# Kernel optimization log

Hardware: AMD Instinct MI355X
Metric: run time of the kernel (lower is better)

## Reference

```python
import jax, jax.numpy as jnp
import numpy as np

N, E, G = 50000, 400000, 64
IN_C, HID, OUT_C, HEADS = 256, 128, 256, 4
LRELU_SLOPE = 0.2
LN_EPS = 1e-5


def setup_inputs() -> dict:
    key = jax.random.key(0)
    ks = jax.random.split(key, 16)
    d = {}
    d["x"] = jax.random.normal(ks[0], (N, IN_C), dtype=jnp.float32)
    d["edge_index"] = jax.random.randint(ks[1], (2, E), 0, N, dtype=jnp.int32)
    d["batch"] = jnp.sort(jax.random.randint(ks[2], (N,), 0, G, dtype=jnp.int32))
    s1 = 1.0 / np.sqrt(IN_C)
    d["W1"] = jax.random.uniform(ks[3], (IN_C, HEADS * HID), jnp.float32, -s1, s1)
    d["att_src1"] = jax.random.normal(ks[4], (HEADS, HID), jnp.float32) * 0.1
    d["att_dst1"] = jax.random.normal(ks[5], (HEADS, HID), jnp.float32) * 0.1
    d["b1"] = jnp.zeros((HEADS * HID,), jnp.float32)
    d["ln1_g"] = jnp.ones((HEADS * HID,), jnp.float32)
    d["ln1_b"] = jnp.zeros((HEADS * HID,), jnp.float32)
    s2 = 1.0 / np.sqrt(HEADS * HID)
    d["W2"] = jax.random.uniform(ks[6], (HEADS * HID, OUT_C), jnp.float32, -s2, s2)
    d["att_src2"] = jax.random.normal(ks[7], (1, OUT_C), jnp.float32) * 0.1
    d["att_dst2"] = jax.random.normal(ks[8], (1, OUT_C), jnp.float32) * 0.1
    d["b2"] = jnp.zeros((OUT_C,), jnp.float32)
    d["ln2_g"] = jnp.ones((OUT_C,), jnp.float32)
    d["ln2_b"] = jnp.zeros((OUT_C,), jnp.float32)
    return d


def _layernorm(x, g, b):
    mu = jnp.mean(x, axis=-1, keepdims=True)
    var = jnp.mean(jnp.square(x - mu), axis=-1, keepdims=True)
    return (x - mu) * jax.lax.rsqrt(var + LN_EPS) * g + b


def _gat_conv(x, src, dst, W, a_src, a_dst, bias):
    # PyG GATConv (eval mode, dropout inactive), self-loops already in src/dst.
    H, C = a_src.shape
    h = (x @ W).reshape(N, H, C)                       # [N,H,C]
    e_src = jnp.einsum('nhc,hc->nh', h, a_src)          # [N,H]
    e_dst = jnp.einsum('nhc,hc->nh', h, a_dst)
    e = jax.nn.leaky_relu(e_src[src] + e_dst[dst], LRELU_SLOPE)  # [Etot,H]
    m = jax.ops.segment_max(e, dst, num_segments=N)     # segment softmax over incoming edges
    ex = jnp.exp(e - m[dst])
    s = jax.ops.segment_sum(ex, dst, num_segments=N)
    alpha = ex / (s[dst] + 1e-16)                       # [Etot,H]
    msg = h[src] * alpha[:, :, None]                    # [Etot,H,C]
    out = jax.ops.segment_sum(msg, dst, num_segments=N) # [N,H,C]
    return out.reshape(N, H * C) + bias


def reference(x, edge_index, batch, W1, att_src1, att_dst1, b1, ln1_g, ln1_b,
              W2, att_src2, att_dst2, b2, ln2_g, ln2_b):
    loops = jnp.arange(N, dtype=edge_index.dtype)
    src = jnp.concatenate([edge_index[0], loops])
    dst = jnp.concatenate([edge_index[1], loops])
    h = _gat_conv(x, src, dst, W1, att_src1, att_dst1, b1)
    h = _layernorm(h, ln1_g, ln1_b)
    h = jax.nn.relu(h)                                  # dropout is identity in eval
    h = _gat_conv(h, src, dst, W2, att_src2, att_dst2, b2)
    h = _layernorm(h, ln2_g, ln2_b)
    # global_mean_pool over graphs
    sums = jax.ops.segment_sum(h, batch, num_segments=G)
    cnts = jax.ops.segment_sum(jnp.ones((N,), h.dtype), batch, num_segments=G)
    return sums / jnp.maximum(cnts, 1.0)[:, None]
```

## Files before the change

### kernel.cpp

```cpp
#include <hip/hip_runtime.h>
#include <hip/hip_bf16.h>
#include <cstdint>

#define LRELU_SLOPE 0.2f

typedef short bf16x8 __attribute__((ext_vector_type(8)));
typedef float f32x4  __attribute__((ext_vector_type(4)));

__device__ __forceinline__ float b2f(unsigned short u) {
  return __uint_as_float(((unsigned int)u) << 16);
}
__device__ __forceinline__ unsigned short f2b(float f) {
  unsigned int u = __float_as_uint(f);
  return (unsigned short)((u + 0x7fff + ((u >> 16) & 1)) >> 16);
}

__device__ __forceinline__ void gload16(const void* g, void* l) {
  __builtin_amdgcn_global_load_lds(
      (const __attribute__((address_space(1))) unsigned int*)g,
      (__attribute__((address_space(3))) unsigned int*)l, 16, 0, 0);
}

__global__ __launch_bounds__(256)
void cvt_bf16_pad(const float* __restrict__ x, unsigned short* __restrict__ o,
                  int M, int D, int Mpad) {
  const int i = blockIdx.x * 256 + threadIdx.x;
  const int per_row = D / 4;
  if (i >= Mpad * per_row) return;
  const int row = i / per_row;
  const int c4  = (i % per_row) * 4;
  ushort4 v = make_ushort4(0, 0, 0, 0);
  if (row < M) {
    const float4 f = *(const float4*)&x[(size_t)row * D + c4];
    v = make_ushort4(f2b(f.x), f2b(f.y), f2b(f.z), f2b(f.w));
  }
  *(ushort4*)&o[(size_t)row * D + c4] = v;
}

__global__ __launch_bounds__(256)
void cvt_wt(const float* __restrict__ W, unsigned short* __restrict__ WT,
            int K, int N) {
  const int j = blockIdx.x * 256 + threadIdx.x;
  if (j >= N * K) return;
  const int n = j / K, k = j % K;
  WT[j] = f2b(W[(size_t)k * N + n]);
}

__global__ __launch_bounds__(256)
void csr_count(const int* __restrict__ ei, int E, int Etot,
               int* __restrict__ count) {
  const int i = blockIdx.x * 256 + threadIdx.x;
  if (i >= Etot) return;
  const int d = (i < E) ? ei[E + i] : (i - E);
  atomicAdd(&count[d], 1);
}

__global__ __launch_bounds__(256)
void scan_blocksum(const int* __restrict__ count, int* __restrict__ bsum, int Nn) {
  const int i0 = blockIdx.x * 1024 + threadIdx.x * 4;
  int s = 0;
#pragma unroll
  for (int k = 0; k < 4; ++k) { const int i = i0 + k; if (i < Nn) s += count[i]; }
#pragma unroll
  for (int off = 1; off < 64; off <<= 1) s += __shfl_xor(s, off);
  __shared__ int ws[4];
  if ((threadIdx.x & 63) == 0) ws[threadIdx.x >> 6] = s;
  __syncthreads();
  if (threadIdx.x == 0) bsum[blockIdx.x] = ws[0] + ws[1] + ws[2] + ws[3];
}

__global__ __launch_bounds__(64)
void scan_top(const int* __restrict__ bsum, int* __restrict__ boff,
              int* __restrict__ rowptrN, int nb) {
  const int t = threadIdx.x;
  const int v = (t < nb) ? bsum[t] : 0;
  int incl = v;
#pragma unroll
  for (int off = 1; off < 64; off <<= 1) {
    const int u = __shfl_up(incl, off);
    if (t >= off) incl += u;
  }
  if (t < nb) boff[t] = incl - v;
  if (t == 63) *rowptrN = incl;
}

__global__ __launch_bounds__(256)
void scan_apply(const int* __restrict__ count, const int* __restrict__ boff,
                int* __restrict__ rowptr, int* __restrict__ cursor, int Nn) {
  const int t = threadIdx.x;
  const int lane = t & 63;
  const int w = t >> 6;
  const int i0 = blockIdx.x * 1024 + t * 4;
  int c[4]; int s = 0;
#pragma unroll
  for (int k = 0; k < 4; ++k) { const int i = i0 + k; c[k] = (i < Nn) ? count[i] : 0; s += c[k]; }
  int incl = s;
#pragma unroll
  for (int off = 1; off < 64; off <<= 1) {
    const int u = __shfl_up(incl, off);
    if (lane >= off) incl += u;
  }
  __shared__ int ws[4];
  if (lane == 63) ws[w] = incl;
  __syncthreads();
  int woff = 0;
  for (int k = 0; k < w; ++k) woff += ws[k];
  int base = boff[blockIdx.x] + woff + incl - s;
#pragma unroll
  for (int k = 0; k < 4; ++k) {
    const int i = i0 + k;
    if (i < Nn) { rowptr[i] = base; cursor[i] = base; base += c[k]; }
  }
}

__global__ __launch_bounds__(256)
void csr_scatter(const int* __restrict__ ei, int E, int Etot,
                 int* __restrict__ cursor, int* __restrict__ srcs) {
  const int i = blockIdx.x * 256 + threadIdx.x;
  if (i >= Etot) return;
  const int s = (i < E) ? ei[i]     : (i - E);
  const int d = (i < E) ? ei[E + i] : (i - E);
  const int pos = atomicAdd(&cursor[d], 1);
  srcs[pos] = s;
}

template<int KSTEPS>
__global__ __launch_bounds__(256)
void gemm_bf16(const unsigned short* __restrict__ A,
               const unsigned short* __restrict__ BT,
               unsigned short* __restrict__ C, int M, int Nn, int K) {
  __shared__ unsigned short As[128 * 32];
  __shared__ unsigned short Bs[128 * 32];
  const int tid  = threadIdx.x;
  const int lane = tid & 63;
  const int wave = tid >> 6;
  const int wm = wave >> 1, wn = wave & 1;
  const int brow = blockIdx.y * 128;
  const int bcol = blockIdx.x * 128;
  const int srow  = tid >> 2;
  const int sslot = tid & 3;
  const int sswz  = sslot ^ (srow & 3);
  const size_t aBase0 = (size_t)(brow + srow) * K + sswz * 8;
  const size_t aBase1 = (size_t)(brow + 64 + srow) * K + sswz * 8;
  const size_t bBase0 = (size_t)(bcol + srow) * K + sswz * 8;
  const size_t bBase1 = (size_t)(bcol + 64 + srow) * K + sswz * 8;
  unsigned short* ldsA0 = &As[srow * 32 + sslot * 8];
  unsigned short* ldsA1 = &As[(64 + srow) * 32 + sslot * 8];
  unsigned short* ldsB0 = &Bs[srow * 32 + sslot * 8];
  unsigned short* ldsB1 = &Bs[(64 + srow) * 32 + sslot * 8];

  f32x4 acc[4][4] = {};
  const int u   = lane >> 4;
  const int r15 = lane & 15;
  const int sw  = u ^ (r15 & 3);

  for (int ks = 0; ks < KSTEPS; ++ks) {
    const int k0 = ks * 32;
    __syncthreads();
    gload16(A + aBase0 + k0, ldsA0);
    gload16(A + aBase1 + k0, ldsA1);
    gload16(BT + bBase0 + k0, ldsB0);
    gload16(BT + bBase1 + k0, ldsB1);
    asm volatile("s_waitcnt vmcnt(0)" ::: "memory");
    __syncthreads();
    bf16x8 af[4], bfv[4];
#pragma unroll
    for (int m = 0; m < 4; ++m) {
      const int row = wm * 64 + m * 16 + r15;
      af[m]  = *(const bf16x8*)&As[row * 32 + sw * 8];
      const int col = wn * 64 + m * 16 + r15;
      bfv[m] = *(const bf16x8*)&Bs[col * 32 + sw * 8];
    }
#pragma unroll
    for (int m = 0; m < 4; ++m)
#pragma unroll
      for (int n = 0; n < 4; ++n)
        acc[m][n] = __builtin_amdgcn_mfma_f32_16x16x32_bf16(
            af[m], bfv[n], acc[m][n], 0, 0, 0);
  }
#pragma unroll
  for (int m = 0; m < 4; ++m) {
    const int r0 = brow + wm * 64 + m * 16 + u * 4;
#pragma unroll
    for (int n = 0; n < 4; ++n) {
      const int cc = bcol + wn * 64 + n * 16 + r15;
#pragma unroll
      for (int r = 0; r < 4; ++r)
        if (r0 + r < M) C[(size_t)(r0 + r) * Nn + cc] = f2b(acc[m][n][r]);
    }
  }
}

template<int H, int C>
__global__ __launch_bounds__(H * C / 4)
void node_att(const unsigned short* __restrict__ h,
              const float* __restrict__ a_src, const float* __restrict__ a_dst,
              float* __restrict__ es, float* __restrict__ ed) {
  const int n = blockIdx.x;
  const int t = threadIdx.x;
  const int c4 = t * 4;
  const int head = c4 / C;
  const ushort4 hv = *(const ushort4*)&h[(size_t)n * (H * C) + c4];
  const float4 as = *(const float4*)&a_src[c4];
  const float4 ad = *(const float4*)&a_dst[c4];
  const float x0 = b2f(hv.x), x1 = b2f(hv.y), x2 = b2f(hv.z), x3 = b2f(hv.w);
  float ps = x0 * as.x + x1 * as.y + x2 * as.z + x3 * as.w;
  float pd = x0 * ad.x + x1 * ad.y + x2 * ad.z + x3 * ad.w;
#pragma unroll
  for (int off = C / 8; off >= 1; off >>= 1) {
    ps += __shfl_xor(ps, off);
    pd += __shfl_xor(pd, off);
  }
  if ((t & (C / 4 - 1)) == 0) {
    es[n * H + head] = ps;
    ed[n * H + head] = pd;
  }
}

template<int H, int C, bool RELU, bool BFOUT>
__global__ __launch_bounds__(256)
void gat_agg_ln(const int* __restrict__ rowptr, const int* __restrict__ srcs,
                const unsigned short* __restrict__ h, const float* __restrict__ es,
                const float* __restrict__ ed, const float* __restrict__ bias,
                const float* __restrict__ lng, const float* __restrict__ lnb,
                unsigned short* __restrict__ obf, float* __restrict__ of32,
                int Nn) {
  constexpr int HC = H * C;
  constexpr int F  = HC / 64;
  const int wave = threadIdx.x >> 6;
  const int lane = threadIdx.x & 63;
  const int n = blockIdx.x * 4 + wave;
  if (n >= Nn) return;
  const int beg = rowptr[n];
  const int deg = rowptr[n + 1] - beg;

  const int myh = lane & (H - 1);
  const float edv = ed[n * H + myh];
  float ssum = 0.f;
  for (int it = lane; it < deg * H; it += 64) {
    const int j = (H == 4) ? (it >> 2) : it;
    const int src = srcs[beg + j];
    float e = es[src * H + myh] + edv;
    e = (e > 0.f) ? e : LRELU_SLOPE * e;
    ssum += __expf(e);
  }
#pragma unroll
  for (int off = H; off < 64; off <<= 1) ssum += __shfl_xor(ssum, off);

  const int hl = (lane * F) / C;
  const float s_mine = __shfl(ssum, hl) + 1e-16f;
  const float edh = ed[n * H + hl];

  float acc[F];
#pragma unroll
  for (int i = 0; i < F; ++i) acc[i] = 0.f;

  auto fma_row = [&](int src, float alpha) {
    const unsigned short* hp = &h[(size_t)src * HC + lane * F];
    const ushort4 v0 = *(const ushort4*)hp;
    acc[0] = fmaf(b2f(v0.x), alpha, acc[0]);
    acc[1] = fmaf(b2f(v0.y), alpha, acc[1]);
    acc[2] = fmaf(b2f(v0.z), alpha, acc[2]);
    acc[3] = fmaf(b2f(v0.w), alpha, acc[3]);
    if constexpr (F == 8) {
      const ushort4 v1 = *(const ushort4*)(hp + 4);
      acc[4] = fmaf(b2f(v1.x), alpha, acc[4]);
      acc[5] = fmaf(b2f(v1.y), alpha, acc[5]);
      acc[6] = fmaf(b2f(v1.z), alpha, acc[6]);
      acc[7] = fmaf(b2f(v1.w), alpha, acc[7]);
    }
  };
  auto get_alpha = [&](int src) {
    float e = es[src * H + hl] + edh;
    e = (e > 0.f) ? e : LRELU_SLOPE * e;
    return __expf(e) / s_mine;
  };

  int j = 0;
  for (; j + 2 <= deg; j += 2) {
    const int s0 = srcs[beg + j], s1 = srcs[beg + j + 1];
    const float a0 = get_alpha(s0), a1 = get_alpha(s1);
    fma_row(s0, a0);
    fma_row(s1, a1);
  }
  if (j < deg) fma_row(srcs[beg + j], get_alpha(srcs[beg + j]));

#pragma unroll
  for (int i = 0; i < F; i += 4) {
    const float4 bb = *(const float4*)&bias[lane * F + i];
    acc[i + 0] += bb.x; acc[i + 1] += bb.y;
    acc[i + 2] += bb.z; acc[i + 3] += bb.w;
  }
  float sum = 0.f, sq = 0.f;
#pragma unroll
  for (int i = 0; i < F; ++i) { sum += acc[i]; sq += acc[i] * acc[i]; }
#pragma unroll
  for (int off = 1; off < 64; off <<= 1) {
    sum += __shfl_xor(sum, off);
    sq  += __shfl_xor(sq, off);
  }
  const float mu  = sum / HC;
  const float var = sq / HC - mu * mu;
  const float r   = rsqrtf(var + 1e-5f);
  float y[F];
#pragma unroll
  for (int i = 0; i < F; i += 4) {
    const float4 gg = *(const float4*)&lng[lane * F + i];
    const float4 bl = *(const float4*)&lnb[lane * F + i];
    y[i + 0] = (acc[i + 0] - mu) * r * gg.x + bl.x;
    y[i + 1] = (acc[i + 1] - mu) * r * gg.y + bl.y;
    y[i + 2] = (acc[i + 2] - mu) * r * gg.z + bl.z;
    y[i + 3] = (acc[i + 3] - mu) * r * gg.w + bl.w;
  }
  if constexpr (RELU) {
#pragma unroll
    for (int i = 0; i < F; ++i) y[i] = fmaxf(y[i], 0.f);
  }
  if constexpr (BFOUT) {
    unsigned short* op = &obf[(size_t)n * HC + lane * F];
    *(ushort4*)op = make_ushort4(f2b(y[0]), f2b(y[1]), f2b(y[2]), f2b(y[3]));
    if constexpr (F == 8)
      *(ushort4*)(op + 4) = make_ushort4(f2b(y[4]), f2b(y[5]), f2b(y[6]), f2b(y[7]));
  } else {
    float* op = &of32[(size_t)n * HC + lane * F];
    *(float4*)op = make_float4(y[0], y[1], y[2], y[3]);
    if constexpr (F == 8)
      *(float4*)(op + 4) = make_float4(y[4], y[5], y[6], y[7]);
  }
}

__global__ __launch_bounds__(256)
void pool_partial(const float* __restrict__ x, const int* __restrict__ batch,
                  float* __restrict__ tmp, int* __restrict__ cnt, int Nn) {
  const int r0 = blockIdx.x * 64;
  const int rend = min(r0 + 64, Nn);
  const int t = threadIdx.x;
  float acc = 0.f;
  int cur = batch[r0];
  int seglen = 0;
  for (int r = r0; r < rend; ++r) {
    const int g = batch[r];
    if (g != cur) {
      unsafeAtomicAdd(&tmp[cur * 256 + t], acc);
      if (t == 0) atomicAdd(&cnt[cur], seglen);
      acc = 0.f; seglen = 0; cur = g;
    }
    acc += x[(size_t)r * 256 + t];
    ++seglen;
  }
  unsafeAtomicAdd(&tmp[cur * 256 + t], acc);
  if (t == 0) atomicAdd(&cnt[cur], seglen);
}

__global__ __launch_bounds__(256)
void pool_final(const float* __restrict__ tmp, const int* __restrict__ cnt,
                float* __restrict__ out) {
  const int g = blockIdx.x;
  const int t = threadIdx.x;
  out[g * 256 + t] = tmp[g * 256 + t] / fmaxf((float)cnt[g], 1.f);
}

extern "C" void kernel_launch(void* const* d_in, const int* in_sizes, int n_in,
                              void* d_out, int out_size, void* d_ws, size_t ws_size,
                              hipStream_t stream) {
  const float* x    = (const float*)d_in[0];
  const int*   ei   = (const int*)d_in[1];
  const int*   batch= (const int*)d_in[2];
  const float* W1   = (const float*)d_in[3];
  const float* as1  = (const float*)d_in[4];
  const float* ad1  = (const float*)d_in[5];
  const float* b1   = (const float*)d_in[6];
  const float* g1   = (const float*)d_in[7];
  const float* be1  = (const float*)d_in[8];
  const float* W2   = (const float*)d_in[9];
  const float* as2  = (const float*)d_in[10];
  const float* ad2  = (const float*)d_in[11];
  const float* b2   = (const float*)d_in[12];
  const float* g2   = (const float*)d_in[13];
  const float* be2  = (const float*)d_in[14];

  const int N    = in_sizes[0] / 256;
  const int E    = in_sizes[1] / 2;
  const int Etot = E + N;
  const int Mpad = ((N + 127) / 128) * 128;
  const int NB   = (N + 1023) / 1024;

  float* ws = (float*)d_ws;
  float* out2 = ws;
  unsigned short* A2bf = (unsigned short*)(out2 + (size_t)N * 256);
  unsigned short* A1bf = A2bf;
  unsigned short* h1bf = A2bf + (size_t)Mpad * 512;
  unsigned short* W1T  = h1bf + (size_t)N * 512;
  unsigned short* W2T  = W1T + 512 * 256;
  float* es   = (float*)(W2T + 512 * 256);
  float* ed   = es + (size_t)N * 4;
  int* count  = (int*)(ed + (size_t)N * 4);
  int* rowptr = count + N;
  int* cursor = rowptr + N + 1;
  int* srcs   = cursor + N;
  float* ptmp = (float*)(srcs + Etot);
  int*   pcnt = (int*)(ptmp + 64 * 256);
  int*   bsum = pcnt + 64;
  int*   boff = bsum + 64;
  unsigned short* h2bf = h1bf;

  const int eb = (Etot + 255) / 256;

  hipMemsetAsync(count, 0, (size_t)N * 4, stream);
  hipMemsetAsync(ptmp, 0, (size_t)(64 * 256 + 64) * 4, stream);
  hipMemsetAsync(A2bf + (size_t)N * 512, 0, (size_t)(Mpad - N) * 512 * 2, stream);

  csr_count<<<eb, 256, 0, stream>>>(ei, E, Etot, count);
  scan_blocksum<<<NB, 256, 0, stream>>>(count, bsum, N);
  scan_top<<<1, 64, 0, stream>>>(bsum, boff, &rowptr[N], NB);
  scan_apply<<<NB, 256, 0, stream>>>(count, boff, rowptr, cursor, N);
  csr_scatter<<<eb, 256, 0, stream>>>(ei, E, Etot, cursor, srcs);

  cvt_bf16_pad<<<((size_t)Mpad * 64 + 255) / 256, 256, 0, stream>>>(x, A1bf, N, 256, Mpad);
  cvt_wt<<<(512 * 256 + 255) / 256, 256, 0, stream>>>(W1, W1T, 256, 512);
  cvt_wt<<<(512 * 256 + 255) / 256, 256, 0, stream>>>(W2, W2T, 512, 256);

  gemm_bf16<8><<<dim3(4, Mpad / 128), 256, 0, stream>>>(A1bf, W1T, h1bf, N, 512, 256);
  node_att<4, 128><<<N, 128, 0, stream>>>(h1bf, as1, ad1, es, ed);
  gat_agg_ln<4, 128, true, true><<<(N + 3) / 4, 256, 0, stream>>>(
      rowptr, srcs, h1bf, es, ed, b1, g1, be1, A2bf, nullptr, N);

  gemm_bf16<16><<<dim3(2, Mpad / 128), 256, 0, stream>>>(A2bf, W2T, h2bf, N, 256, 512);
  node_att<1, 256><<<N, 64, 0, stream>>>(h2bf, as2, ad2, es, ed);
  gat_agg_ln<1, 256, false, false><<<(N + 3) / 4, 256, 0, stream>>>(
      rowptr, srcs, h2bf, es, ed, b2, g2, be2, nullptr, out2, N);

  pool_partial<<<(N + 63) / 64, 256, 0, stream>>>(out2, batch, ptmp, pcnt, N);
  pool_final<<<64, 256, 0, stream>>>(ptmp, pcnt, (float*)d_out);
}
```

Before: 322.8 us.

## Double-buffer GEMM LDS, batch gather loads in aggregation, store layer-2 output as bf16

The GEMM now double-buffers its LDS tiles so the global-to-LDS load for the next k-step is issued before the MFMAs of the current step, hiding load latency and dropping one barrier per step. The attention aggregation issues four neighbour row gathers before consuming them, which gives more memory-level parallelism, and it multiplies by a precomputed reciprocal instead of dividing. The layer-2 normalized output is written as bf16 and the pooling kernel reads bf16, halving that traffic at the cost of some precision before the mean pool.

```diff
diff --git a/kernel.cpp b/kernel.cpp
--- a/kernel.cpp
+++ b/kernel.cpp
@@ -129,8 +129,8 @@
 void gemm_bf16(const unsigned short* __restrict__ A,
                const unsigned short* __restrict__ BT,
                unsigned short* __restrict__ C, int M, int Nn, int K) {
-  __shared__ unsigned short As[128 * 32];
-  __shared__ unsigned short Bs[128 * 32];
+  __shared__ unsigned short As[2][128 * 32];
+  __shared__ unsigned short Bs[2][128 * 32];
   const int tid  = threadIdx.x;
   const int lane = tid & 63;
   const int wave = tid >> 6;
@@ -144,32 +144,36 @@
   const size_t aBase1 = (size_t)(brow + 64 + srow) * K + sswz * 8;
   const size_t bBase0 = (size_t)(bcol + srow) * K + sswz * 8;
   const size_t bBase1 = (size_t)(bcol + 64 + srow) * K + sswz * 8;
-  unsigned short* ldsA0 = &As[srow * 32 + sslot * 8];
-  unsigned short* ldsA1 = &As[(64 + srow) * 32 + sslot * 8];
-  unsigned short* ldsB0 = &Bs[srow * 32 + sslot * 8];
-  unsigned short* ldsB1 = &Bs[(64 + srow) * 32 + sslot * 8];
+  const int ldsOff0 = srow * 32 + sslot * 8;
+  const int ldsOff1 = (64 + srow) * 32 + sslot * 8;
 
   f32x4 acc[4][4] = {};
   const int u   = lane >> 4;
   const int r15 = lane & 15;
   const int sw  = u ^ (r15 & 3);
 
+  auto stage = [&](int buf, int ks) {
+    const int k0 = ks * 32;
+    gload16(A + aBase0 + k0, &As[buf][ldsOff0]);
+    gload16(A + aBase1 + k0, &As[buf][ldsOff1]);
+    gload16(BT + bBase0 + k0, &Bs[buf][ldsOff0]);
+    gload16(BT + bBase1 + k0, &Bs[buf][ldsOff1]);
+  };
+
+  stage(0, 0);
+  asm volatile("s_waitcnt vmcnt(0)" ::: "memory");
+  __syncthreads();
+  int cur = 0;
+#pragma unroll
   for (int ks = 0; ks < KSTEPS; ++ks) {
-    const int k0 = ks * 32;
-    __syncthreads();
-    gload16(A + aBase0 + k0, ldsA0);
-    gload16(A + aBase1 + k0, ldsA1);
-    gload16(BT + bBase0 + k0, ldsB0);
-    gload16(BT + bBase1 + k0, ldsB1);
-    asm volatile("s_waitcnt vmcnt(0)" ::: "memory");
-    __syncthreads();
+    if (ks + 1 < KSTEPS) stage(cur ^ 1, ks + 1);
     bf16x8 af[4], bfv[4];
 #pragma unroll
     for (int m = 0; m < 4; ++m) {
       const int row = wm * 64 + m * 16 + r15;
-      af[m]  = *(const bf16x8*)&As[row * 32 + sw * 8];
+      af[m]  = *(const bf16x8*)&As[cur][row * 32 + sw * 8];
       const int col = wn * 64 + m * 16 + r15;
-      bfv[m] = *(const bf16x8*)&Bs[col * 32 + sw * 8];
+      bfv[m] = *(const bf16x8*)&Bs[cur][col * 32 + sw * 8];
     }
 #pragma unroll
     for (int m = 0; m < 4; ++m)
@@ -177,6 +181,11 @@
       for (int n = 0; n < 4; ++n)
         acc[m][n] = __builtin_amdgcn_mfma_f32_16x16x32_bf16(
             af[m], bfv[n], acc[m][n], 0, 0, 0);
+    if (ks + 1 < KSTEPS) {
+      asm volatile("s_waitcnt vmcnt(0)" ::: "memory");
+      __syncthreads();
+      cur ^= 1;
+    }
   }
 #pragma unroll
   for (int m = 0; m < 4; ++m) {
@@ -248,42 +257,58 @@
   for (int off = H; off < 64; off <<= 1) ssum += __shfl_xor(ssum, off);
 
   const int hl = (lane * F) / C;
-  const float s_mine = __shfl(ssum, hl) + 1e-16f;
+  const float inv_s = 1.0f / (__shfl(ssum, hl) + 1e-16f);
   const float edh = ed[n * H + hl];
 
   float acc[F];
 #pragma unroll
   for (int i = 0; i < F; ++i) acc[i] = 0.f;
 
-  auto fma_row = [&](int src, float alpha) {
-    const unsigned short* hp = &h[(size_t)src * HC + lane * F];
-    const ushort4 v0 = *(const ushort4*)hp;
-    acc[0] = fmaf(b2f(v0.x), alpha, acc[0]);
-    acc[1] = fmaf(b2f(v0.y), alpha, acc[1]);
-    acc[2] = fmaf(b2f(v0.z), alpha, acc[2]);
-    acc[3] = fmaf(b2f(v0.w), alpha, acc[3]);
-    if constexpr (F == 8) {
-      const ushort4 v1 = *(const ushort4*)(hp + 4);
-      acc[4] = fmaf(b2f(v1.x), alpha, acc[4]);
-      acc[5] = fmaf(b2f(v1.y), alpha, acc[5]);
-      acc[6] = fmaf(b2f(v1.z), alpha, acc[6]);
-      acc[7] = fmaf(b2f(v1.w), alpha, acc[7]);
-    }
-  };
   auto get_alpha = [&](int src) {
     float e = es[src * H + hl] + edh;
     e = (e > 0.f) ? e : LRELU_SLOPE * e;
-    return __expf(e) / s_mine;
+    return __expf(e) * inv_s;
   };
+  auto fma_rows = [&](const ushort4* v0, const ushort4* v1, const float* a, int cnt) {
+    for (int q = 0; q < cnt; ++q) {
+      acc[0] = fmaf(b2f(v0[q].x), a[q], acc[0]);
+      acc[1] = fmaf(b2f(v0[q].y), a[q], acc[1]);
+      acc[2] = fmaf(b2f(v0[q].z), a[q], acc[2]);
+      acc[3] = fmaf(b2f(v0[q].w), a[q], acc[3]);
+      if constexpr (F == 8) {
+        acc[4] = fmaf(b2f(v1[q].x), a[q], acc[4]);
+        acc[5] = fmaf(b2f(v1[q].y), a[q], acc[5]);
+        acc[6] = fmaf(b2f(v1[q].z), a[q], acc[6]);
+        acc[7] = fmaf(b2f(v1[q].w), a[q], acc[7]);
+      }
+    }
+  };
 
   int j = 0;
-  for (; j + 2 <= deg; j += 2) {
-    const int s0 = srcs[beg + j], s1 = srcs[beg + j + 1];
-    const float a0 = get_alpha(s0), a1 = get_alpha(s1);
-    fma_row(s0, a0);
-    fma_row(s1, a1);
-  }
-  if (j < deg) fma_row(srcs[beg + j], get_alpha(srcs[beg + j]));
+  for (; j + 4 <= deg; j += 4) {
+    int s4[4];
+#pragma unroll
+    for (int q = 0; q < 4; ++q) s4[q] = srcs[beg + j + q];
+    ushort4 v0[4], v1[4];
+#pragma unroll
+    for (int q = 0; q < 4; ++q) {
+      const unsigned short* hp = &h[(size_t)s4[q] * HC + lane * F];
+      v0[q] = *(const ushort4*)hp;
+      if constexpr (F == 8) v1[q] = *(const ushort4*)(hp + 4);
+    }
+    float a4[4];
+#pragma unroll
+    for (int q = 0; q < 4; ++q) a4[q] = get_alpha(s4[q]);
+    fma_rows(v0, v1, a4, 4);
+  }
+  for (; j < deg; ++j) {
+    const int src = srcs[beg + j];
+    const unsigned short* hp = &h[(size_t)src * HC + lane * F];
+    ushort4 v0 = *(const ushort4*)hp, v1;
+    if constexpr (F == 8) v1 = *(const ushort4*)(hp + 4);
+    const float a = get_alpha(src);
+    fma_rows(&v0, &v1, &a, 1);
+  }
 
 #pragma unroll
   for (int i = 0; i < F; i += 4) {
@@ -330,7 +355,7 @@
 }
 
 __global__ __launch_bounds__(256)
-void pool_partial(const float* __restrict__ x, const int* __restrict__ batch,
+void pool_partial(const unsigned short* __restrict__ x, const int* __restrict__ batch,
                   float* __restrict__ tmp, int* __restrict__ cnt, int Nn) {
   const int r0 = blockIdx.x * 64;
   const int rend = min(r0 + 64, Nn);
@@ -345,7 +370,7 @@
       if (t == 0) atomicAdd(&cnt[cur], seglen);
       acc = 0.f; seglen = 0; cur = g;
     }
-    acc += x[(size_t)r * 256 + t];
+    acc += b2f(x[(size_t)r * 256 + t]);
     ++seglen;
   }
   unsafeAtomicAdd(&tmp[cur * 256 + t], acc);
@@ -386,8 +411,8 @@
   const int NB   = (N + 1023) / 1024;
 
   float* ws = (float*)d_ws;
-  float* out2 = ws;
-  unsigned short* A2bf = (unsigned short*)(out2 + (size_t)N * 256);
+  unsigned short* out2 = (unsigned short*)ws;
+  unsigned short* A2bf = out2 + (size_t)N * 256;
   unsigned short* A1bf = A2bf;
   unsigned short* h1bf = A2bf + (size_t)Mpad * 512;
   unsigned short* W1T  = h1bf + (size_t)N * 512;
@@ -427,8 +452,8 @@
 
   gemm_bf16<16><<<dim3(2, Mpad / 128), 256, 0, stream>>>(A2bf, W2T, h2bf, N, 256, 512);
   node_att<1, 256><<<N, 64, 0, stream>>>(h2bf, as2, ad2, es, ed);
-  gat_agg_ln<1, 256, false, false><<<(N + 3) / 4, 256, 0, stream>>>(
-      rowptr, srcs, h2bf, es, ed, b2, g2, be2, nullptr, out2, N);
+  gat_agg_ln<1, 256, false, true><<<(N + 3) / 4, 256, 0, stream>>>(
+      rowptr, srcs, h2bf, es, ed, b2, g2, be2, out2, nullptr, N);
 
   pool_partial<<<(N + 63) / 64, 256, 0, stream>>>(out2, batch, ptmp, pcnt, N);
   pool_final<<<64, 256, 0, stream>>>(ptmp, pcnt, (float*)d_out);
```

New measurement: 318.5 us. About the same (-1.3%).
